# Performance work log

Hardware: AMD Instinct MI355X
Metric: run time of the kernel (lower is better)

Reference implementation:

```python
import jax, jax.numpy as jnp
import numpy as np

B, T, D = 8, 16384, 128


def setup_inputs() -> dict:
    key = jax.random.key(0)
    ks = jax.random.split(key, 14)
    sc = lambda fan_in: 1.0 / np.sqrt(fan_in)
    x = jax.random.normal(ks[0], (B, T, D), jnp.float32)
    return {
        "x": x,
        # BindingField (scale 0): bind_key / bind_query Linear(D, D//2)
        "Wk": jax.random.normal(ks[1], (D, D // 2), jnp.float32) * sc(D),
        "bk": jnp.zeros((D // 2,), jnp.float32),
        "Wq": jax.random.normal(ks[2], (D, D // 2), jnp.float32) * sc(D),
        "bq": jnp.zeros((D // 2,), jnp.float32),
        # aggregator (scale 0): Linear(D,D) -> LayerNorm(D) -> ReLU -> Linear(D,D)
        "Wa1": jax.random.normal(ks[3], (D, D), jnp.float32) * sc(D),
        "ba1": jnp.zeros((D,), jnp.float32),
        "ln_g": jnp.ones((D,), jnp.float32),
        "ln_b": jnp.zeros((D,), jnp.float32),
        "Wa2": jax.random.normal(ks[4], (D, D), jnp.float32) * sc(D),
        "ba2": jnp.zeros((D,), jnp.float32),
        # downward_influence (scale 0): Linear(D,D)
        "Wd": jax.random.normal(ks[5], (D, D), jnp.float32) * sc(D),
        "bd": jnp.zeros((D,), jnp.float32),
    }


def reference(x, Wk, bk, Wq, bq, Wa1, ba1, ln_g, ln_b, Wa2, ba2, Wd, bd):
    Bn, Tn, Dn = x.shape
    BIND_THRESHOLD = 0.5
    LN_EPS = 1e-5

    # ---- BindingField: binding strength between adjacent tokens ----
    keys = x[:, :-1] @ Wk + bk                       # [B, T-1, D/2]
    queries = x[:, 1:] @ Wq + bq                     # [B, T-1, D/2]
    strength = jax.nn.sigmoid((keys * queries).sum(-1) / float(np.sqrt(Dn // 2)))
    bind = strength > BIND_THRESHOLD                 # [B, T-1]

    # chunk_starts: token 0 always starts; token t starts iff NOT bound to t-1
    chunk_starts = jnp.concatenate([jnp.ones((Bn, 1), bool), ~bind], axis=1)
    seg = jnp.cumsum(chunk_starts.astype(jnp.int32), axis=1) - 1  # [B, T] chunk id per token

    # ---- aggregate_chunks: ragged mean-pool via segment_sum (pad to T chunk slots) ----
    seg_flat = (seg + jnp.arange(Bn, dtype=jnp.int32)[:, None] * Tn).reshape(-1)
    sums = jax.ops.segment_sum(x.reshape(-1, Dn), seg_flat, num_segments=Bn * Tn)
    counts = jax.ops.segment_sum(jnp.ones((Bn * Tn,), x.dtype), seg_flat,
                                 num_segments=Bn * Tn)
    chunk_mean = (sums / jnp.maximum(counts, 1.0)[:, None]).reshape(Bn, Tn, Dn)

    # aggregator MLP: Linear -> LayerNorm -> ReLU -> Linear
    h = chunk_mean @ Wa1 + ba1
    mu = h.mean(-1, keepdims=True)
    var = ((h - mu) ** 2).mean(-1, keepdims=True)    # biased var, as torch LayerNorm
    h = (h - mu) * jax.lax.rsqrt(var + LN_EPS) * ln_g + ln_b
    agg = jax.nn.relu(h) @ Wa2 + ba2                 # [B, T(chunk slots), D]

    # ---- apply_downward_influence: broadcast chunk signal back to its tokens ----
    infl = agg @ Wd + bd                             # [B, T(chunks), D]
    gathered = jnp.take_along_axis(infl, seg[..., None].astype(jnp.int32), axis=1)
    gate = jax.nn.sigmoid(gathered)
    return x * gate + x
```

## Files before the change

### kernel.cpp

```cpp
#include <hip/hip_runtime.h>
#include <math.h>

#define BB 8
#define TT 16384
#define DD 128
#define DH 64
#define FCAP 32768
#define FMARGIN 0.05f

typedef _Float16 half8 __attribute__((ext_vector_type(8)));
typedef float f32x4 __attribute__((ext_vector_type(4)));

union H8 { half8 h; uint4 q; ushort us[8]; };

static __device__ __forceinline__ float4 ld4(const float* p) { return *(const float4*)p; }

static __device__ __forceinline__ uint pk2(float a, float b) {
    union { _Float16 f; ushort u; } A, B;
    A.f = (_Float16)a; B.f = (_Float16)b;
    return (uint)A.u | ((uint)B.u << 16);
}

static __device__ __forceinline__ void split8h(const float4 v0, const float4 v1,
                                               half8* xh, half8* xl)
{
    float f[8] = {v0.x, v0.y, v0.z, v0.w, v1.x, v1.y, v1.z, v1.w};
    half8 h, l;
    #pragma unroll
    for (int j = 0; j < 8; ++j) {
        _Float16 hv = (_Float16)f[j];
        h[j] = hv;
        l[j] = (_Float16)(f[j] - (float)hv);
    }
    *xh = h; *xl = l;
}

__global__ __launch_bounds__(64) void k_wprep(
    const float* __restrict__ Wa1, const float* __restrict__ Wa2,
    const float* __restrict__ Wd, const float* __restrict__ Wk,
    const float* __restrict__ Wq, ushort* __restrict__ wfm,
    ushort* __restrict__ wfb, int* __restrict__ fcnt)
{
    const int l  = threadIdx.x;
    const int nt = blockIdx.x & 7;
    const int kb = blockIdx.x >> 3;
    const int ly = blockIdx.y;
    if (ly == 0 && blockIdx.x == 0 && l == 0) *fcnt = 0;
    const int n  = nt * 16 + (l & 15);
    const int k0 = kb * 32 + (l >> 4) * 8;
    H8 v;
    if (ly < 3) {
        const float* W = (ly == 0) ? Wa1 : (ly == 1) ? Wa2 : Wd;
        #pragma unroll
        for (int e = 0; e < 8; ++e) v.h[e] = (_Float16)W[(k0 + e) * DD + n];
        *(uint4*)(wfm + (size_t)(((ly * 8 + nt) * 4 + kb) * 64 + l) * 8) = v.q;
    } else {
        #pragma unroll
        for (int e = 0; e < 8; ++e) {
            float w = (n < 64) ? Wk[(k0 + e) * DH + n] : Wq[(k0 + e) * DH + n - 64];
            v.h[e] = (_Float16)w;
        }
        *(uint4*)(wfb + (size_t)((nt * 4 + kb) * 64 + l) * 8) = v.q;
    }
}

__global__ __launch_bounds__(256, 2) void k_bind(
    const float* __restrict__ x, const ushort* __restrict__ wfb,
    const float* __restrict__ bk, const float* __restrict__ bq,
    int* __restrict__ cstart, int* __restrict__ flist, int* __restrict__ fcnt)
{
    __shared__ uint4 Bs4[2048];
    __shared__ float bnd[4][64];
    const int b    = blockIdx.y;
    const int tb   = blockIdx.x * 64;
    const int tid  = threadIdx.x;
    const int wv   = tid >> 6;
    const int l    = tid & 63;
    const int lo16 = l & 15;
    const int g    = l >> 4;

    {
        const uint4* wsrc = (const uint4*)wfb;
        #pragma unroll
        for (int j = 0; j < 8; ++j) { int idx = tid + j * 256; Bs4[idx] = wsrc[idx]; }
    }

    const float* xrow = x + ((size_t)b * TT + tb + wv * 16 + lo16) * DD;
    half8 xh[4], xl[4];
    #pragma unroll
    for (int kb = 0; kb < 4; ++kb) {
        float4 v0 = ld4(xrow + kb * 32 + g * 8);
        float4 v1 = ld4(xrow + kb * 32 + g * 8 + 4);
        split8h(v0, v1, &xh[kb], &xl[kb]);
    }
    int r64 = tb + 64; if (r64 > TT - 1) r64 = TT - 1;
    const float* xq = x + ((size_t)b * TT + r64) * DD;
    half8 qh[4], ql[4];
    H8 z; z.q.x = z.q.y = z.q.z = z.q.w = 0u;
    #pragma unroll
    for (int kb = 0; kb < 4; ++kb) {
        qh[kb] = z.h; ql[kb] = z.h;
        if (lo16 == 0) {
            float4 v0 = ld4(xq + kb * 32 + g * 8);
            float4 v1 = ld4(xq + kb * 32 + g * 8 + 4);
            split8h(v0, v1, &qh[kb], &ql[kb]);
        }
    }

    f32x4 acc[8];
    #pragma unroll
    for (int nt = 0; nt < 8; ++nt) {
        int col = nt * 16 + lo16;
        float bias = (col < 64) ? bk[col] : bq[col - 64];
        acc[nt] = (f32x4){bias, bias, bias, bias};
    }
    f32x4 acc4;
    {
        float bias = bq[wv * 16 + lo16];
        acc4 = (f32x4){bias, bias, bias, bias};
    }

    __syncthreads();
    const ushort* Bs = (const ushort*)Bs4;
    const ushort* Bs_halo = Bs + (size_t)((4 + wv) * 4 * 64 + l) * 8;
    #pragma unroll
    for (int kb = 0; kb < 4; ++kb) {
        half8 bh[8];
        #pragma unroll
        for (int nt = 0; nt < 8; ++nt)
            bh[nt] = *(const half8*)(Bs + (size_t)((nt * 4 + kb) * 64 + l) * 8);
        #pragma unroll
        for (int nt = 0; nt < 8; ++nt) {
            acc[nt] = __builtin_amdgcn_mfma_f32_16x16x32_f16(xh[kb], bh[nt], acc[nt], 0, 0, 0);
            acc[nt] = __builtin_amdgcn_mfma_f32_16x16x32_f16(xl[kb], bh[nt], acc[nt], 0, 0, 0);
        }
        half8 bh4 = *(const half8*)(Bs_halo + (size_t)kb * 64 * 8);
        acc4 = __builtin_amdgcn_mfma_f32_16x16x32_f16(qh[kb], bh4, acc4, 0, 0, 0);
        acc4 = __builtin_amdgcn_mfma_f32_16x16x32_f16(ql[kb], bh4, acc4, 0, 0, 0);
    }

    if (l < 16) {
        if (wv > 0) {
            #pragma unroll
            for (int nt = 0; nt < 4; ++nt) bnd[wv - 1][nt * 16 + lo16] = acc[4 + nt][0];
        }
        bnd[3][wv * 16 + lo16] = acc4[0];
    }
    __syncthreads();

    float qn3[4];
    #pragma unroll
    for (int nt = 0; nt < 4; ++nt) qn3[nt] = __shfl_down(acc[4 + nt][0], 16);
    if (g == 3) {
        #pragma unroll
        for (int nt = 0; nt < 4; ++nt) qn3[nt] = bnd[wv][nt * 16 + lo16];
    }
    float s[4];
    #pragma unroll
    for (int i = 0; i < 3; ++i) {
        float t = 0.f;
        #pragma unroll
        for (int nt = 0; nt < 4; ++nt) t += acc[nt][i] * acc[4 + nt][i + 1];
        s[i] = t;
    }
    {
        float t = 0.f;
        #pragma unroll
        for (int nt = 0; nt < 4; ++nt) t += acc[nt][3] * qn3[nt];
        s[3] = t;
    }
    #pragma unroll
    for (int i = 0; i < 4; ++i) {
        #pragma unroll
        for (int m = 1; m < 16; m <<= 1) s[i] += __shfl_xor(s[i], m);
    }
    if (lo16 == 0) {
        #pragma unroll
        for (int i = 0; i < 4; ++i) {
            int t = tb + wv * 16 + g * 4 + i;
            if (t <= TT - 2) {
                cstart[b * TT + t + 1] = (s[i] > 0.f) ? 0 : 1;
                if (fabsf(s[i]) < FMARGIN) {
                    int pos = atomicAdd(fcnt, 1);
                    if (pos < FCAP) flist[pos] = b * TT + t;
                }
            }
        }
    }
    if (blockIdx.x == 0 && tid == 0) cstart[b * TT] = 1;
}

__global__ __launch_bounds__(256) void k_fixup(
    const float* __restrict__ x, const float* __restrict__ Wk, const float* __restrict__ bk,
    const float* __restrict__ Wq, const float* __restrict__ bq,
    const int* __restrict__ flist, const int* __restrict__ fcnt, int* __restrict__ cstart)
{
    const int n    = min(*fcnt, FCAP);
    const int wv   = (blockIdx.x * 256 + threadIdx.x) >> 6;
    const int lane = threadIdx.x & 63;
    const int nwv  = gridDim.x * 4;
    for (int i = wv; i < n; i += nwv) {
        int idx = flist[i];
        int b = idx >> 14;
        int t = idx & (TT - 1);
        const float* xt = x + ((size_t)b * TT + t) * DD;
        float K = bk[lane], Q = bq[lane];
        #pragma unroll 8
        for (int k = 0; k < DD; ++k) {
            K = fmaf(xt[k],      Wk[k * DH + lane], K);
            Q = fmaf(xt[DD + k], Wq[k * DH + lane], Q);
        }
        float p = K * Q;
        #pragma unroll
        for (int m = 1; m < 64; m <<= 1) p += __shfl_xor(p, m);
        if (lane == 0) cstart[b * TT + t + 1] = (p > 0.f) ? 0 : 1;
    }
}

__global__ __launch_bounds__(1024) void k_scan(const int* __restrict__ cstart,
    int* __restrict__ seg, int* __restrict__ cs, int* __restrict__ numC)
{
    __shared__ int wsum[16];
    const int b = blockIdx.x, tid = threadIdx.x;
    const int wv = tid >> 6, lane = tid & 63;
    const int base = b * TT + tid * 16;
    int v[16];
    #pragma unroll
    for (int i = 0; i < 4; ++i) {
        int4 q = *(const int4*)(cstart + base + i * 4);
        v[i * 4 + 0] = q.x; v[i * 4 + 1] = q.y; v[i * 4 + 2] = q.z; v[i * 4 + 3] = q.w;
    }
    int s[16]; int run = 0;
    #pragma unroll
    for (int i = 0; i < 16; ++i) { run += v[i]; s[i] = run; }
    int incl = run;
    #pragma unroll
    for (int off = 1; off < 64; off <<= 1) {
        int t = __shfl_up(incl, off);
        if (lane >= off) incl += t;
    }
    if (lane == 63) wsum[wv] = incl;
    __syncthreads();
    if (tid < 16) {
        int w = wsum[tid];
        #pragma unroll
        for (int off = 1; off < 16; off <<= 1) {
            int t = __shfl_up(w, off, 16);
            if (tid >= off) w += t;
        }
        wsum[tid] = w;
    }
    __syncthreads();
    const int excl = (wv ? wsum[wv - 1] : 0) + incl - run;
    #pragma unroll
    for (int i = 0; i < 16; ++i) {
        int sg = excl + s[i] - 1;
        seg[base + i] = sg;
        if (v[i]) cs[b * (TT + 1) + sg] = tid * 16 + i;
    }
    if (tid == 1023) {
        int tot = excl + run;
        numC[b] = tot;
        cs[b * (TT + 1) + tot] = TT;
    }
}

__device__ __forceinline__ void mlp_gemm(f32x4 acc[8], const uint4* Afr4,
    const ushort* Bs, int wv, int l)
{
    half8 af[4];
    #pragma unroll
    for (int kb = 0; kb < 4; ++kb)
        af[kb] = *(const half8*)((const char*)Afr4 + ((wv * 4 + kb) * 64 + l) * 16);
    #pragma unroll
    for (int kb = 0; kb < 4; ++kb) {
        half8 bh[8];
        #pragma unroll
        for (int nt = 0; nt < 8; ++nt)
            bh[nt] = *(const half8*)(Bs + (size_t)((nt * 4 + kb) * 64 + l) * 8);
        #pragma unroll
        for (int nt = 0; nt < 8; ++nt)
            acc[nt] = __builtin_amdgcn_mfma_f32_16x16x32_f16(af[kb], bh[nt], acc[nt], 0, 0, 0);
    }
}

__global__ __launch_bounds__(256, 2) void k_mlp(
    const float* __restrict__ x, const int* __restrict__ cs,
    const float* __restrict__ ba1, const float* __restrict__ ln_g, const float* __restrict__ ln_b,
    const float* __restrict__ ba2, const float* __restrict__ bd,
    const ushort* __restrict__ wfm, const int* __restrict__ numC, float* __restrict__ cm)
{
    __shared__ uint4 Afr4[1024];
    __shared__ uint4 Bs4[2048];
    const int b  = blockIdx.y;
    const int nC = numC[b];
    const int c0 = blockIdx.x * 64;
    if (c0 >= nC) return;
    const int tid  = threadIdx.x;
    const int wv   = tid >> 6;
    const int l    = tid & 63;
    const int lo16 = l & 15;
    const int g    = l >> 4;
    const ushort* Bs = (const ushort*)Bs4;
    const uint4* wsrc = (const uint4*)wfm;

    #pragma unroll
    for (int j = 0; j < 8; ++j) { int idx = tid + j * 256; Bs4[idx] = wsrc[idx]; }

    for (int i = tid; i < 64 * 32; i += 256) {
        int r = i >> 5, c4 = (i & 31) * 4;
        float4 sv = make_float4(0.f, 0.f, 0.f, 0.f);
        int c = c0 + r;
        if (c < nC) {
            int t0 = cs[b * (TT + 1) + c], t1 = cs[b * (TT + 1) + c + 1];
            const float* xp = x + ((size_t)b * TT + t0) * DD + c4;
            for (int t = t0; t < t1; ++t, xp += DD) {
                float4 v = ld4(xp);
                sv.x += v.x; sv.y += v.y; sv.z += v.z; sv.w += v.w;
            }
            float inv = 1.f / (float)(t1 - t0);
            sv.x *= inv; sv.y *= inv; sv.z *= inv; sv.w *= inv;
        }
        int frag = (r >> 4) * 4 + (c4 >> 5);
        int lane = (r & 15) + (((c4 & 31) >> 3) * 16);
        uint2 pk = make_uint2(pk2(sv.x, sv.y), pk2(sv.z, sv.w));
        *(uint2*)((char*)Afr4 + frag * 1024 + lane * 16 + (c4 & 7) * 2) = pk;
    }
    __syncthreads();

    f32x4 acc[8];
    #pragma unroll
    for (int nt = 0; nt < 8; ++nt) {
        float bias = ba1[nt * 16 + lo16];
        acc[nt] = (f32x4){bias, bias, bias, bias};
    }
    mlp_gemm(acc, Afr4, Bs, wv, l);

    float mu_[4], rs_[4];
    #pragma unroll
    for (int i = 0; i < 4; ++i) {
        float sm = 0.f;
        #pragma unroll
        for (int nt = 0; nt < 8; ++nt) sm += acc[nt][i];
        #pragma unroll
        for (int k = 1; k < 16; k <<= 1) sm += __shfl_xor(sm, k, 16);
        mu_[i] = sm * (1.f / 128.f);
        float vs = 0.f;
        #pragma unroll
        for (int nt = 0; nt < 8; ++nt) { float d = acc[nt][i] - mu_[i]; vs += d * d; }
        #pragma unroll
        for (int k = 1; k < 16; k <<= 1) vs += __shfl_xor(vs, k, 16);
        rs_[i] = rsqrtf(vs * (1.f / 128.f) + 1e-5f);
    }
    float gam[8], bet[8];
    #pragma unroll
    for (int nt = 0; nt < 8; ++nt) { gam[nt] = ln_g[nt * 16 + lo16]; bet[nt] = ln_b[nt * 16 + lo16]; }

    __syncthreads();
    #pragma unroll
    for (int nt = 0; nt < 8; ++nt) {
        int cw = nt * 16 + lo16;
        int frag = wv * 4 + (cw >> 5);
        int lnf  = (((cw & 31) >> 3) * 16);
        #pragma unroll
        for (int i = 0; i < 4; ++i) {
            float h = fmaf((acc[nt][i] - mu_[i]) * rs_[i], gam[nt], bet[nt]);
            union { _Float16 f; ushort u; } cv; cv.f = (_Float16)fmaxf(h, 0.f);
            *((ushort*)((char*)Afr4 + frag * 1024 + ((g * 4 + i) + lnf) * 16 + (cw & 7) * 2)) = cv.u;
        }
    }
    #pragma unroll
    for (int j = 0; j < 8; ++j) { int idx = tid + j * 256; Bs4[idx] = wsrc[2048 + idx]; }
    __syncthreads();

    #pragma unroll
    for (int nt = 0; nt < 8; ++nt) {
        float bias = ba2[nt * 16 + lo16];
        acc[nt] = (f32x4){bias, bias, bias, bias};
    }
    mlp_gemm(acc, Afr4, Bs, wv, l);
    __syncthreads();
    #pragma unroll
    for (int nt = 0; nt < 8; ++nt) {
        int cw = nt * 16 + lo16;
        int frag = wv * 4 + (cw >> 5);
        int lnf  = (((cw & 31) >> 3) * 16);
        #pragma unroll
        for (int i = 0; i < 4; ++i) {
            union { _Float16 f; ushort u; } cv; cv.f = (_Float16)acc[nt][i];
            *((ushort*)((char*)Afr4 + frag * 1024 + ((g * 4 + i) + lnf) * 16 + (cw & 7) * 2)) = cv.u;
        }
    }
    #pragma unroll
    for (int j = 0; j < 8; ++j) { int idx = tid + j * 256; Bs4[idx] = wsrc[4096 + idx]; }
    __syncthreads();

    #pragma unroll
    for (int nt = 0; nt < 8; ++nt) {
        float bias = bd[nt * 16 + lo16];
        acc[nt] = (f32x4){bias, bias, bias, bias};
    }
    mlp_gemm(acc, Afr4, Bs, wv, l);
    #pragma unroll
    for (int i = 0; i < 4; ++i) {
        int row = c0 + wv * 16 + g * 4 + i;
        if (row < nC) {
            float* dst = cm + ((size_t)b * TT + row) * DD + lo16;
            #pragma unroll
            for (int nt = 0; nt < 8; ++nt)
                dst[nt * 16] = 1.f / (1.f + __expf(-acc[nt][i]));
        }
    }
}

__global__ __launch_bounds__(256) void k_out(const float* __restrict__ x,
    const int* __restrict__ seg, const float* __restrict__ gate, float* __restrict__ out)
{
    const size_t idx = (size_t)blockIdx.x * 256 + threadIdx.x;
    const size_t tok = idx >> 5;
    const int d4 = (int)(idx & 31);
    const int b  = (int)(tok >> 14);
    const int sg = seg[tok];
    float4 gv = ld4(gate + (((size_t)b << 14) + sg) * DD + d4 * 4);
    float4 xv = ld4(x + tok * DD + (size_t)d4 * 4);
    float4 o;
    o.x = fmaf(xv.x, gv.x, xv.x);
    o.y = fmaf(xv.y, gv.y, xv.y);
    o.z = fmaf(xv.z, gv.z, xv.z);
    o.w = fmaf(xv.w, gv.w, xv.w);
    *(float4*)(out + idx * 4) = o;
}

extern "C" void kernel_launch(void* const* d_in, const int* in_sizes, int n_in,
                              void* d_out, int out_size, void* d_ws, size_t ws_size,
                              hipStream_t stream)
{
    (void)in_sizes; (void)n_in; (void)out_size; (void)ws_size;
    const float* x    = (const float*)d_in[0];
    const float* Wk   = (const float*)d_in[1];
    const float* bk   = (const float*)d_in[2];
    const float* Wq   = (const float*)d_in[3];
    const float* bq   = (const float*)d_in[4];
    const float* Wa1  = (const float*)d_in[5];
    const float* ba1  = (const float*)d_in[6];
    const float* ln_g = (const float*)d_in[7];
    const float* ln_b = (const float*)d_in[8];
    const float* Wa2  = (const float*)d_in[9];
    const float* ba2  = (const float*)d_in[10];
    const float* Wd   = (const float*)d_in[11];
    const float* bd   = (const float*)d_in[12];
    float* out = (float*)d_out;

    char* p = (char*)d_ws;
    float* cm    = (float*)p;   p += (size_t)BB * TT * DD * 4;
    int* seg     = (int*)p;     p += (size_t)BB * TT * 4;
    int* cs      = (int*)p;     p += (size_t)BB * (TT + 1) * 4;
    int* numC    = (int*)p;     p += 64;
    ushort* wfm  = (ushort*)p;  p += 3 * DD * DD * 2;
    ushort* wfb  = (ushort*)p;  p += DD * DD * 2;
    int* flist   = (int*)p;     p += (size_t)FCAP * 4;
    int* fcnt    = (int*)p;

    k_wprep<<<dim3(32, 4), 64, 0, stream>>>(Wa1, Wa2, Wd, Wk, Wq, wfm, wfb, fcnt);
    k_bind<<<dim3(256, BB), 256, 0, stream>>>(x, wfb, bk, bq, seg, flist, fcnt);
    k_fixup<<<dim3(256), 256, 0, stream>>>(x, Wk, bk, Wq, bq, flist, fcnt, seg);
    k_scan<<<dim3(BB), 1024, 0, stream>>>(seg, seg, cs, numC);
    k_mlp<<<dim3(TT / 64, BB), 256, 0, stream>>>(x, cs, ba1, ln_g, ln_b, ba2, bd, wfm, numC, cm);
    k_out<<<dim3(BB * TT * DD / (256 * 4)), 256, 0, stream>>>(x, seg, cm, out);
}
```

Measured before the change: 121.4 us.

## Pool chunk sums via token-parallel LDS atomics instead of per-chunk serial loops

The chunk mean-pool in the MLP kernel used to have each thread walk all tokens of one chunk serially, so a long chunk left one thread doing all the work. Now all threads stride over the block's token range with coalesced float4 loads and accumulate into a zeroed padded LDS accumulator with shared-memory atomics. The results are then divided by the counts and packed into the fp16 fragment layout. This balances work across threads but adds an LDS zeroing pass, atomic contention when chunks are long, extra barriers and a larger shared footprint that may reduce occupancy.

```diff
diff --git a/kernel.cpp b/kernel.cpp
--- a/kernel.cpp
+++ b/kernel.cpp
@@ -285,12 +285,12 @@
 }
 
 __global__ __launch_bounds__(256, 2) void k_mlp(
-    const float* __restrict__ x, const int* __restrict__ cs,
+    const float* __restrict__ x, const int* __restrict__ cs, const int* __restrict__ seg,
     const float* __restrict__ ba1, const float* __restrict__ ln_g, const float* __restrict__ ln_b,
     const float* __restrict__ ba2, const float* __restrict__ bd,
     const ushort* __restrict__ wfm, const int* __restrict__ numC, float* __restrict__ cm)
 {
-    __shared__ uint4 Afr4[1024];
+    __shared__ union { float Acc[64 * 132]; uint4 Afr4[1024]; } smA;
     __shared__ uint4 Bs4[2048];
     const int b  = blockIdx.y;
     const int nC = numC[b];
@@ -307,24 +307,56 @@
     #pragma unroll
     for (int j = 0; j < 8; ++j) { int idx = tid + j * 256; Bs4[idx] = wsrc[idx]; }
 
-    for (int i = tid; i < 64 * 32; i += 256) {
+    {
+        float4 z4 = make_float4(0.f, 0.f, 0.f, 0.f);
+        for (int i = tid; i < 64 * 132 / 4; i += 256) ((float4*)smA.Acc)[i] = z4;
+    }
+    __syncthreads();
+
+    {
+        const int base = b * (TT + 1) + c0;
+        const int T0 = cs[base];
+        const int cEnd = (c0 + 64 < nC) ? (c0 + 64) : nC;
+        const int T1 = cs[b * (TT + 1) + cEnd];
+        const int nw = (T1 - T0) * 32;
+        for (int jj = tid; jj < nw; jj += 256) {
+            int tok = T0 + (jj >> 5);
+            int d4  = (jj & 31) * 4;
+            float4 v = ld4(x + ((size_t)b * TT + tok) * DD + d4);
+            int row = seg[b * TT + tok] - c0;
+            float* ap = &smA.Acc[row * 132 + d4];
+            atomicAdd(ap + 0, v.x);
+            atomicAdd(ap + 1, v.y);
+            atomicAdd(ap + 2, v.z);
+            atomicAdd(ap + 3, v.w);
+        }
+    }
+    __syncthreads();
+
+    float4 vals[8];
+    #pragma unroll
+    for (int ii = 0; ii < 8; ++ii) {
+        int i = tid + ii * 256;
         int r = i >> 5, c4 = (i & 31) * 4;
+        int c = c0 + r;
         float4 sv = make_float4(0.f, 0.f, 0.f, 0.f);
-        int c = c0 + r;
         if (c < nC) {
             int t0 = cs[b * (TT + 1) + c], t1 = cs[b * (TT + 1) + c + 1];
-            const float* xp = x + ((size_t)b * TT + t0) * DD + c4;
-            for (int t = t0; t < t1; ++t, xp += DD) {
-                float4 v = ld4(xp);
-                sv.x += v.x; sv.y += v.y; sv.z += v.z; sv.w += v.w;
-            }
             float inv = 1.f / (float)(t1 - t0);
-            sv.x *= inv; sv.y *= inv; sv.z *= inv; sv.w *= inv;
-        }
+            const float* ap = &smA.Acc[r * 132 + c4];
+            sv.x = ap[0] * inv; sv.y = ap[1] * inv; sv.z = ap[2] * inv; sv.w = ap[3] * inv;
+        }
+        vals[ii] = sv;
+    }
+    __syncthreads();
+    #pragma unroll
+    for (int ii = 0; ii < 8; ++ii) {
+        int i = tid + ii * 256;
+        int r = i >> 5, c4 = (i & 31) * 4;
         int frag = (r >> 4) * 4 + (c4 >> 5);
-        int lane = (r & 15) + (((c4 & 31) >> 3) * 16);
-        uint2 pk = make_uint2(pk2(sv.x, sv.y), pk2(sv.z, sv.w));
-        *(uint2*)((char*)Afr4 + frag * 1024 + lane * 16 + (c4 & 7) * 2) = pk;
+        int lanef = (r & 15) + (((c4 & 31) >> 3) * 16);
+        uint2 pk = make_uint2(pk2(vals[ii].x, vals[ii].y), pk2(vals[ii].z, vals[ii].w));
+        *(uint2*)((char*)smA.Afr4 + frag * 1024 + lanef * 16 + (c4 & 7) * 2) = pk;
     }
     __syncthreads();
 
@@ -334,7 +366,7 @@
         float bias = ba1[nt * 16 + lo16];
         acc[nt] = (f32x4){bias, bias, bias, bias};
     }
-    mlp_gemm(acc, Afr4, Bs, wv, l);
+    mlp_gemm(acc, smA.Afr4, Bs, wv, l);
 
     float mu_[4], rs_[4];
     #pragma unroll
@@ -366,7 +398,7 @@
         for (int i = 0; i < 4; ++i) {
             float h = fmaf((acc[nt][i] - mu_[i]) * rs_[i], gam[nt], bet[nt]);
             union { _Float16 f; ushort u; } cv; cv.f = (_Float16)fmaxf(h, 0.f);
-            *((ushort*)((char*)Afr4 + frag * 1024 + ((g * 4 + i) + lnf) * 16 + (cw & 7) * 2)) = cv.u;
+            *((ushort*)((char*)smA.Afr4 + frag * 1024 + ((g * 4 + i) + lnf) * 16 + (cw & 7) * 2)) = cv.u;
         }
     }
     #pragma unroll
@@ -378,7 +410,7 @@
         float bias = ba2[nt * 16 + lo16];
         acc[nt] = (f32x4){bias, bias, bias, bias};
     }
-    mlp_gemm(acc, Afr4, Bs, wv, l);
+    mlp_gemm(acc, smA.Afr4, Bs, wv, l);
     __syncthreads();
     #pragma unroll
     for (int nt = 0; nt < 8; ++nt) {
@@ -388,7 +420,7 @@
         #pragma unroll
         for (int i = 0; i < 4; ++i) {
             union { _Float16 f; ushort u; } cv; cv.f = (_Float16)acc[nt][i];
-            *((ushort*)((char*)Afr4 + frag * 1024 + ((g * 4 + i) + lnf) * 16 + (cw & 7) * 2)) = cv.u;
+            *((ushort*)((char*)smA.Afr4 + frag * 1024 + ((g * 4 + i) + lnf) * 16 + (cw & 7) * 2)) = cv.u;
         }
     }
     #pragma unroll
@@ -400,7 +432,7 @@
         float bias = bd[nt * 16 + lo16];
         acc[nt] = (f32x4){bias, bias, bias, bias};
     }
-    mlp_gemm(acc, Afr4, Bs, wv, l);
+    mlp_gemm(acc, smA.Afr4, Bs, wv, l);
     #pragma unroll
     for (int i = 0; i < 4; ++i) {
         int row = c0 + wv * 16 + g * 4 + i;
@@ -465,6 +497,6 @@
     k_bind<<<dim3(256, BB), 256, 0, stream>>>(x, wfb, bk, bq, seg, flist, fcnt);
     k_fixup<<<dim3(256), 256, 0, stream>>>(x, Wk, bk, Wq, bq, flist, fcnt, seg);
     k_scan<<<dim3(BB), 1024, 0, stream>>>(seg, seg, cs, numC);
-    k_mlp<<<dim3(TT / 64, BB), 256, 0, stream>>>(x, cs, ba1, ln_g, ln_b, ba2, bd, wfm, numC, cm);
+    k_mlp<<<dim3(TT / 64, BB), 256, 0, stream>>>(x, cs, seg, ba1, ln_g, ln_b, ba2, bd, wfm, numC, cm);
     k_out<<<dim3(BB * TT * DD / (256 * 4)), 256, 0, stream>>>(x, seg, cm, out);
 }
```

After: 220.8 us. 82.0% more time.

## Stage chunk token rows through shared memory with coalesced loads before mean-pooling

Applied to the files above, without the earlier changes.

The chunk mean-pooling in the MLP kernel now covers the whole contiguous token range of the block's 64 chunks. It loads that range in 64-token tiles into a padded shared-memory buffer with coalesced float4 loads, then each thread accumulates its chunk/column slice from LDS. Before, each thread walked its own chunk's tokens straight from global memory. The shared buffer is unioned with the fragment and weight buffers to keep the LDS footprint bounded. The cost is extra barriers per tile, more registers for per-thread accumulators and bounds, and load imbalance when chunk lengths vary.

```diff
diff --git a/kernel.cpp b/kernel.cpp
--- a/kernel.cpp
+++ b/kernel.cpp
@@ -290,8 +290,10 @@
     const float* __restrict__ ba2, const float* __restrict__ bd,
     const ushort* __restrict__ wfm, const int* __restrict__ numC, float* __restrict__ cm)
 {
-    __shared__ uint4 Afr4[1024];
-    __shared__ uint4 Bs4[2048];
+    __shared__ union {
+        float Tok[64 * 132];
+        struct { uint4 Afr[1024]; uint4 Bs[2048]; } fb;
+    } sm;
     const int b  = blockIdx.y;
     const int nC = numC[b];
     const int c0 = blockIdx.x * 64;
@@ -301,31 +303,65 @@
     const int l    = tid & 63;
     const int lo16 = l & 15;
     const int g    = l >> 4;
-    const ushort* Bs = (const ushort*)Bs4;
+    const ushort* Bs = (const ushort*)sm.fb.Bs;
     const uint4* wsrc = (const uint4*)wfm;
 
-    #pragma unroll
-    for (int j = 0; j < 8; ++j) { int idx = tid + j * 256; Bs4[idx] = wsrc[idx]; }
-
-    for (int i = tid; i < 64 * 32; i += 256) {
+    const int cbase = b * (TT + 1);
+    const int T0 = cs[cbase + c0];
+    const int cEnd = (c0 + 64 < nC) ? (c0 + 64) : nC;
+    const int T1 = cs[cbase + cEnd];
+    int t0r[8], t1r[8];
+    #pragma unroll
+    for (int ii = 0; ii < 8; ++ii) {
+        int r = (tid + ii * 256) >> 5;
+        int c = c0 + r;
+        t0r[ii] = (c < nC) ? cs[cbase + c] : 0;
+        t1r[ii] = (c < nC) ? cs[cbase + c + 1] : 0;
+    }
+    float4 vals[8];
+    #pragma unroll
+    for (int ii = 0; ii < 8; ++ii) vals[ii] = make_float4(0.f, 0.f, 0.f, 0.f);
+
+    for (int tt = T0; tt < T1; tt += 64) {
+        __syncthreads();
+        const int tEnd = (tt + 64 < T1) ? (tt + 64) : T1;
+        for (int j = tid; j < (tEnd - tt) * 32; j += 256) {
+            int trow = j >> 5, c4 = (j & 31) * 4;
+            *(float4*)&sm.Tok[trow * 132 + c4] =
+                ld4(x + ((size_t)b * TT + tt + trow) * DD + c4);
+        }
+        __syncthreads();
+        #pragma unroll
+        for (int ii = 0; ii < 8; ++ii) {
+            int c4 = ((tid + ii * 256) & 31) * 4;
+            int lo = (t0r[ii] > tt)   ? t0r[ii] : tt;
+            int hi = (t1r[ii] < tEnd) ? t1r[ii] : tEnd;
+            for (int t = lo; t < hi; ++t) {
+                const float* ap = &sm.Tok[(t - tt) * 132 + c4];
+                vals[ii].x += ap[0]; vals[ii].y += ap[1];
+                vals[ii].z += ap[2]; vals[ii].w += ap[3];
+            }
+        }
+    }
+    __syncthreads();
+
+    #pragma unroll
+    for (int ii = 0; ii < 8; ++ii) {
+        int i = tid + ii * 256;
         int r = i >> 5, c4 = (i & 31) * 4;
         float4 sv = make_float4(0.f, 0.f, 0.f, 0.f);
-        int c = c0 + r;
-        if (c < nC) {
-            int t0 = cs[b * (TT + 1) + c], t1 = cs[b * (TT + 1) + c + 1];
-            const float* xp = x + ((size_t)b * TT + t0) * DD + c4;
-            for (int t = t0; t < t1; ++t, xp += DD) {
-                float4 v = ld4(xp);
-                sv.x += v.x; sv.y += v.y; sv.z += v.z; sv.w += v.w;
-            }
-            float inv = 1.f / (float)(t1 - t0);
-            sv.x *= inv; sv.y *= inv; sv.z *= inv; sv.w *= inv;
+        if (c0 + r < nC) {
+            float inv = 1.f / (float)(t1r[ii] - t0r[ii]);
+            sv.x = vals[ii].x * inv; sv.y = vals[ii].y * inv;
+            sv.z = vals[ii].z * inv; sv.w = vals[ii].w * inv;
         }
         int frag = (r >> 4) * 4 + (c4 >> 5);
-        int lane = (r & 15) + (((c4 & 31) >> 3) * 16);
+        int lanef = (r & 15) + (((c4 & 31) >> 3) * 16);
         uint2 pk = make_uint2(pk2(sv.x, sv.y), pk2(sv.z, sv.w));
-        *(uint2*)((char*)Afr4 + frag * 1024 + lane * 16 + (c4 & 7) * 2) = pk;
-    }
+        *(uint2*)((char*)sm.fb.Afr + frag * 1024 + lanef * 16 + (c4 & 7) * 2) = pk;
+    }
+    #pragma unroll
+    for (int j = 0; j < 8; ++j) { int idx = tid + j * 256; sm.fb.Bs[idx] = wsrc[idx]; }
     __syncthreads();
 
     f32x4 acc[8];
@@ -334,17 +370,17 @@
         float bias = ba1[nt * 16 + lo16];
         acc[nt] = (f32x4){bias, bias, bias, bias};
     }
-    mlp_gemm(acc, Afr4, Bs, wv, l);
+    mlp_gemm(acc, sm.fb.Afr, Bs, wv, l);
 
     float mu_[4], rs_[4];
     #pragma unroll
     for (int i = 0; i < 4; ++i) {
-        float sm = 0.f;
-        #pragma unroll
-        for (int nt = 0; nt < 8; ++nt) sm += acc[nt][i];
-        #pragma unroll
-        for (int k = 1; k < 16; k <<= 1) sm += __shfl_xor(sm, k, 16);
-        mu_[i] = sm * (1.f / 128.f);
+        float smv = 0.f;
+        #pragma unroll
+        for (int nt = 0; nt < 8; ++nt) smv += acc[nt][i];
+        #pragma unroll
+        for (int k = 1; k < 16; k <<= 1) smv += __shfl_xor(smv, k, 16);
+        mu_[i] = smv * (1.f / 128.f);
         float vs = 0.f;
         #pragma unroll
         for (int nt = 0; nt < 8; ++nt) { float d = acc[nt][i] - mu_[i]; vs += d * d; }
@@ -366,11 +402,11 @@
         for (int i = 0; i < 4; ++i) {
             float h = fmaf((acc[nt][i] - mu_[i]) * rs_[i], gam[nt], bet[nt]);
             union { _Float16 f; ushort u; } cv; cv.f = (_Float16)fmaxf(h, 0.f);
-            *((ushort*)((char*)Afr4 + frag * 1024 + ((g * 4 + i) + lnf) * 16 + (cw & 7) * 2)) = cv.u;
-        }
-    }
-    #pragma unroll
-    for (int j = 0; j < 8; ++j) { int idx = tid + j * 256; Bs4[idx] = wsrc[2048 + idx]; }
+            *((ushort*)((char*)sm.fb.Afr + frag * 1024 + ((g * 4 + i) + lnf) * 16 + (cw & 7) * 2)) = cv.u;
+        }
+    }
+    #pragma unroll
+    for (int j = 0; j < 8; ++j) { int idx = tid + j * 256; sm.fb.Bs[idx] = wsrc[2048 + idx]; }
     __syncthreads();
 
     #pragma unroll
@@ -378,7 +414,7 @@
         float bias = ba2[nt * 16 + lo16];
         acc[nt] = (f32x4){bias, bias, bias, bias};
     }
-    mlp_gemm(acc, Afr4, Bs, wv, l);
+    mlp_gemm(acc, sm.fb.Afr, Bs, wv, l);
     __syncthreads();
     #pragma unroll
     for (int nt = 0; nt < 8; ++nt) {
@@ -388,11 +424,11 @@
         #pragma unroll
         for (int i = 0; i < 4; ++i) {
             union { _Float16 f; ushort u; } cv; cv.f = (_Float16)acc[nt][i];
-            *((ushort*)((char*)Afr4 + frag * 1024 + ((g * 4 + i) + lnf) * 16 + (cw & 7) * 2)) = cv.u;
-        }
-    }
-    #pragma unroll
-    for (int j = 0; j < 8; ++j) { int idx = tid + j * 256; Bs4[idx] = wsrc[4096 + idx]; }
+            *((ushort*)((char*)sm.fb.Afr + frag * 1024 + ((g * 4 + i) + lnf) * 16 + (cw & 7) * 2)) = cv.u;
+        }
+    }
+    #pragma unroll
+    for (int j = 0; j < 8; ++j) { int idx = tid + j * 256; sm.fb.Bs[idx] = wsrc[4096 + idx]; }
     __syncthreads();
 
     #pragma unroll
@@ -400,7 +436,7 @@
         float bias = bd[nt * 16 + lo16];
         acc[nt] = (f32x4){bias, bias, bias, bias};
     }
-    mlp_gemm(acc, Afr4, Bs, wv, l);
+    mlp_gemm(acc, sm.fb.Afr, Bs, wv, l);
     #pragma unroll
     for (int i = 0; i < 4; ++i) {
         int row = c0 + wv * 16 + g * 4 + i;
```

After: 118.2 us. 2.6% less time.
